# Kernel optimization log

Measured on AMD Instinct MI355X. Metric: run time of the kernel, lower is better.

Reference implementation:

```python
import jax, jax.numpy as jnp
import numpy as np

B, C, H, W = 4, 64, 64, 64
RATIO = 8  # channel reduction in the channel-attention branch
C8 = C // RATIO


def conv1x1(x, Wt, b):
    # 1x1 conv == channel-mixing matmul. Wt: (out_c, in_c), x: (B, in_c, H, W)
    return jnp.einsum('oc,bchw->bohw', Wt, x) + b[None, :, None, None]


def setup_inputs() -> dict:
    key = jax.random.key(0)
    ks = jax.random.split(key, 12)
    s = 0.02
    return {
        'x': jax.random.normal(ks[0], (B, C, H, W), dtype=jnp.float32),
        'y': jax.random.normal(ks[1], (B, C, H, W), dtype=jnp.float32),
        'Wq': jax.random.normal(ks[2], (C, C), dtype=jnp.float32) * s,
        'bq': jnp.zeros((C,), dtype=jnp.float32),
        'Wk': jax.random.normal(ks[3], (C, C), dtype=jnp.float32) * s,
        'bk': jnp.zeros((C,), dtype=jnp.float32),
        'Wv': jax.random.normal(ks[4], (C, C), dtype=jnp.float32) * s,
        'bv': jnp.zeros((C,), dtype=jnp.float32),
        'Wq1': jax.random.normal(ks[5], (C8, C), dtype=jnp.float32) * s,
        'bq1': jnp.zeros((C8,), dtype=jnp.float32),
        'Wk1': jax.random.normal(ks[6], (C8, C), dtype=jnp.float32) * s,
        'bk1': jnp.zeros((C8,), dtype=jnp.float32),
    }


def reference(x, y, Wq, bq, Wk, bk, Wv, bv, Wq1, bq1, Wk1, bk1):
    b, c, h, w = x.shape
    hw = h * w
    # cross-attention branch: query from y, key/value from x
    Q = conv1x1(y, Wq, bq).reshape(b, c, hw)   # (B, C, HW)
    K = conv1x1(x, Wk, bk).reshape(b, c, hw)
    V = conv1x1(x, Wv, bv).reshape(b, c, hw)
    attn = jax.nn.softmax(jnp.einsum('bcq,bck->bqk', Q, K), axis=-1)  # (B, HW, HW)
    # channel-attention branch (PAM-style spatial map from x, ratio 8)
    Q1 = conv1x1(x, Wq1, bq1).reshape(b, C8, hw)
    K1 = conv1x1(x, Wk1, bk1).reshape(b, C8, hw)
    attn1 = jax.nn.softmax(jnp.einsum('bcq,bck->bqk', Q1, K1), axis=-1)  # (B, HW, HW)
    # out = attn @ V^T + attn1 @ V^T, shape (B, HW, C)
    out = jnp.einsum('bqk,bck->bqc', attn, V) + jnp.einsum('bqk,bck->bqc', attn1, V)
    return out.transpose(0, 2, 1).reshape(b, c, h, w)
```

## Files before the change

kernel.cpp:

```cpp
#include <hip/hip_runtime.h>
#include <hip/hip_bf16.h>


typedef __bf16 bf16x8 __attribute__((ext_vector_type(8)));
typedef float f32x16 __attribute__((ext_vector_type(16)));

#define MFMA32(A, B, C) __builtin_amdgcn_mfma_f32_32x32x16_bf16((A), (B), (C), 0, 0, 0)

#define LOG2E 1.4426950408889634f
#define EXP2F(x) __builtin_amdgcn_exp2f(x)

__device__ __forceinline__ uint4 ld16(const unsigned short* p) {
  return *reinterpret_cast<const uint4*>(p);
}
__device__ __forceinline__ bf16x8 asbf(uint4 v) {
  return __builtin_bit_cast(bf16x8, v);
}
__device__ __forceinline__ unsigned short f2bf(float f) {
  return __builtin_bit_cast(unsigned short, __float2bfloat16(f));
}
__device__ __forceinline__ unsigned cvtpk(float a, float b) {
  unsigned r;
  asm("v_cvt_pk_bf16_f32 %0, %1, %2" : "=v"(r) : "v"(a), "v"(b));
  return r;
}

__global__ __launch_bounds__(256) void proj_kernel(
    const float* __restrict__ x, const float* __restrict__ y,
    const float* __restrict__ Wq, const float* __restrict__ bq,
    const float* __restrict__ Wk, const float* __restrict__ bk,
    const float* __restrict__ Wv, const float* __restrict__ bv,
    const float* __restrict__ Wq1, const float* __restrict__ bq1,
    const float* __restrict__ Wk1, const float* __restrict__ bk1,
    unsigned short* __restrict__ Qb, unsigned short* __restrict__ Kb,
    unsigned short* __restrict__ VtT, unsigned short* __restrict__ Q1c,
    unsigned short* __restrict__ K1c)
{
  __shared__ float ldsT[64][32];
  __shared__ float ldsW[64][65];
  __shared__ float ldsW2[64][65];
  __shared__ float ldsW1[8][64];
  __shared__ float ldsW1b[8][64];

  const int t = threadIdx.x;
  const int b = blockIdx.x >> 7;
  const int p0 = (blockIdx.x & 127) << 5;
  const int lane = t & 63;
  const int w = t >> 6;

  for (int i = t; i < 2048; i += 256) {
    int c = i >> 5, p = i & 31;
    ldsT[c][p] = y[(size_t)(b * 64 + c) * 4096 + p0 + p];
  }
  for (int i = t; i < 4096; i += 256) {
    int c = i >> 6, p = i & 63;
    ldsW[c][p] = Wq[i];
    ldsW2[c][p] = Wv[i];
  }
  for (int i = t; i < 512; i += 256) {
    ldsW1[i >> 6][i & 63] = Wq1[i];
    ldsW1b[i >> 6][i & 63] = Wk1[i];
  }
  __syncthreads();

  {
    float acc[8];
    float bias = bq[lane];
#pragma unroll
    for (int pp = 0; pp < 8; ++pp) acc[pp] = bias;
    for (int ic = 0; ic < 64; ++ic) {
      float wv_ = ldsW[lane][ic];
#pragma unroll
      for (int pp = 0; pp < 8; ++pp)
        acc[pp] = fmaf(wv_, ldsT[ic][w * 8 + pp], acc[pp]);
    }
#pragma unroll
    for (int pp = 0; pp < 8; ++pp)
      Qb[(size_t)(b * 4096 + p0 + w * 8 + pp) * 64 + lane] = f2bf(acc[pp] * LOG2E);
  }
  __syncthreads();

  for (int i = t; i < 2048; i += 256) {
    int c = i >> 5, p = i & 31;
    ldsT[c][p] = x[(size_t)(b * 64 + c) * 4096 + p0 + p];
  }
  for (int i = t; i < 4096; i += 256) {
    int c = i >> 6, p = i & 63;
    ldsW[c][p] = Wk[i];
  }
  __syncthreads();

  {
    float acc[8];
    float bias = bk[lane];
#pragma unroll
    for (int pp = 0; pp < 8; ++pp) acc[pp] = bias;
    for (int ic = 0; ic < 64; ++ic) {
      float wv_ = ldsW[lane][ic];
#pragma unroll
      for (int pp = 0; pp < 8; ++pp)
        acc[pp] = fmaf(wv_, ldsT[ic][w * 8 + pp], acc[pp]);
    }
#pragma unroll
    for (int pp = 0; pp < 8; ++pp)
      Kb[(size_t)(b * 4096 + p0 + w * 8 + pp) * 64 + lane] = f2bf(acc[pp]);
  }

  {
    const int half = lane >> 5;
    const int px = lane & 31;
    const int oc0 = 16 * w + 8 * half;
    float acc[8];
#pragma unroll
    for (int j = 0; j < 8; ++j) acc[j] = bv[oc0 + j];
    for (int ic = 0; ic < 64; ++ic) {
      float xv = ldsT[ic][px];
#pragma unroll
      for (int j = 0; j < 8; ++j)
        acc[j] = fmaf(ldsW2[oc0 + j][ic], xv, acc[j]);
    }
    const int k = p0 + px;
    const int kblk = k >> 5, ki = k & 31;
#pragma unroll
    for (int j = 0; j < 8; ++j)
      VtT[((size_t)(b * 128 + kblk) * 64 + oc0 + j) * 32 + ki] = f2bf(acc[j]);
  }

  if (w == 0 && lane < 32) {
    float acc[8];
#pragma unroll
    for (int j = 0; j < 8; ++j) acc[j] = bq1[j];
    for (int ic = 0; ic < 64; ++ic) {
      float xv = ldsT[ic][lane];
#pragma unroll
      for (int j = 0; j < 8; ++j)
        acc[j] = fmaf(ldsW1[j][ic], xv, acc[j]);
    }
    uint4 o;
    o.x = cvtpk(acc[0] * LOG2E, acc[1] * LOG2E);
    o.y = cvtpk(acc[2] * LOG2E, acc[3] * LOG2E);
    o.z = cvtpk(acc[4] * LOG2E, acc[5] * LOG2E);
    o.w = cvtpk(acc[6] * LOG2E, acc[7] * LOG2E);
    *reinterpret_cast<uint4*>(Q1c + (size_t)(b * 4096 + p0 + lane) * 8) = o;
  } else if (w == 1 && lane < 32) {
    float acc[8];
#pragma unroll
    for (int j = 0; j < 8; ++j) acc[j] = bk1[j];
    for (int ic = 0; ic < 64; ++ic) {
      float xv = ldsT[ic][lane];
#pragma unroll
      for (int j = 0; j < 8; ++j)
        acc[j] = fmaf(ldsW1b[j][ic], xv, acc[j]);
    }
    uint4 o;
    o.x = cvtpk(acc[0], acc[1]); o.y = cvtpk(acc[2], acc[3]);
    o.z = cvtpk(acc[4], acc[5]); o.w = cvtpk(acc[6], acc[7]);
    *reinterpret_cast<uint4*>(K1c + (size_t)(b * 4096 + p0 + lane) * 8) = o;
  }
}

__global__ __launch_bounds__(512, 2) void attn_kernel(
    const unsigned short* __restrict__ Qb, const unsigned short* __restrict__ Kb,
    const unsigned short* __restrict__ VtT, const unsigned short* __restrict__ Q1c,
    const unsigned short* __restrict__ K1c, float* __restrict__ out)
{
  __shared__ float accbuf[2][2][64][32];
  __shared__ float zbuf[8][2][32];

  const int id = blockIdx.x;
  const int b = (id & 7) >> 1;
  const int qt = (id >> 3) + ((id & 1) << 6);
  const int q0 = qt * 32;

  const int wid = threadIdx.x >> 6;
  const int l = threadIdx.x & 63;
  const int qc = l & 31;
  const int h = l >> 5;

  const int kBeg = wid << 9;
  const int kEnd = kBeg + 512;

  const f32x16 zero16 = {0.f,0.f,0.f,0.f, 0.f,0.f,0.f,0.f,
                         0.f,0.f,0.f,0.f, 0.f,0.f,0.f,0.f};
  const uint4 zu4 = {0u, 0u, 0u, 0u};

  const unsigned short* qrow = Qb + (size_t)(b * 4096 + q0 + qc) * 64 + 8 * h;
  bf16x8 qf[4];
#pragma unroll
  for (int m = 0; m < 4; ++m) qf[m] = asbf(ld16(qrow + 16 * m));
  bf16x8 q1f;
  {
    uint4 v = zu4;
    if (h == 0) v = ld16(Q1c + (size_t)(b * 4096 + q0 + qc) * 8);
    q1f = asbf(v);
  }

  f32x16 accA0 = zero16, accA1 = zero16, accB0 = zero16, accB1 = zero16;
  float zA = 0.f, zB = 0.f;

#pragma unroll 1
  for (int k0 = kBeg; k0 < kEnd; k0 += 32) {
    uint4 kf[4], vf[4], k1f;
    {
      const unsigned short* kp = Kb + ((size_t)(b * 4096 + k0 + qc) << 6) + 8 * h;
      kf[0] = ld16(kp);
      kf[1] = ld16(kp + 16);
      kf[2] = ld16(kp + 32);
      kf[3] = ld16(kp + 48);
      k1f = zu4;
      if (h == 0) k1f = ld16(K1c + (size_t)(b * 4096 + k0 + qc) * 8);
      const unsigned short* vp =
          VtT + (((size_t)(b * 128 + (k0 >> 5)) * 64 + qc) << 5) + 8 * h;
      vf[0] = ld16(vp);
      vf[1] = ld16(vp + 16);
      vf[2] = ld16(vp + 32 * 32);
      vf[3] = ld16(vp + 32 * 32 + 16);
    }

    __builtin_amdgcn_s_setprio(1);
    f32x16 sD = MFMA32(asbf(kf[0]), qf[0], zero16);
    sD = MFMA32(asbf(kf[1]), qf[1], sD);
    sD = MFMA32(asbf(kf[2]), qf[2], sD);
    sD = MFMA32(asbf(kf[3]), qf[3], sD);
    f32x16 uD = MFMA32(asbf(k1f), q1f, zero16);
    __builtin_amdgcn_s_setprio(0);

#pragma unroll
    for (int r = 0; r < 16; ++r) { sD[r] = EXP2F(sD[r]); uD[r] = EXP2F(uD[r]); }
    zA += (((sD[0]+sD[1])+(sD[2]+sD[3])) + ((sD[4]+sD[5])+(sD[6]+sD[7]))) +
          (((sD[8]+sD[9])+(sD[10]+sD[11])) + ((sD[12]+sD[13])+(sD[14]+sD[15])));
    zB += (((uD[0]+uD[1])+(uD[2]+uD[3])) + ((uD[4]+uD[5])+(uD[6]+uD[7]))) +
          (((uD[8]+uD[9])+(uD[10]+uD[11])) + ((uD[12]+uD[13])+(uD[14]+uD[15])));

#pragma unroll
    for (int m = 0; m < 2; ++m) {
      unsigned W0 = cvtpk(sD[8*m+0], sD[8*m+1]);
      unsigned W1 = cvtpk(sD[8*m+2], sD[8*m+3]);
      unsigned W2 = cvtpk(sD[8*m+4], sD[8*m+5]);
      unsigned W3 = cvtpk(sD[8*m+6], sD[8*m+7]);
      auto s1 = __builtin_amdgcn_permlane32_swap((int)W0, (int)W2, false, false);
      auto s2 = __builtin_amdgcn_permlane32_swap((int)W1, (int)W3, false, false);
      uint4 pw;
      pw.x = (unsigned)s1[0]; pw.y = (unsigned)s2[0];
      pw.z = (unsigned)s1[1]; pw.w = (unsigned)s2[1];
      bf16x8 pf = asbf(pw);

      unsigned X0 = cvtpk(uD[8*m+0], uD[8*m+1]);
      unsigned X1 = cvtpk(uD[8*m+2], uD[8*m+3]);
      unsigned X2 = cvtpk(uD[8*m+4], uD[8*m+5]);
      unsigned X3 = cvtpk(uD[8*m+6], uD[8*m+7]);
      auto t1 = __builtin_amdgcn_permlane32_swap((int)X0, (int)X2, false, false);
      auto t2 = __builtin_amdgcn_permlane32_swap((int)X1, (int)X3, false, false);
      uint4 pw1;
      pw1.x = (unsigned)t1[0]; pw1.y = (unsigned)t2[0];
      pw1.z = (unsigned)t1[1]; pw1.w = (unsigned)t2[1];
      bf16x8 pf1 = asbf(pw1);

      __builtin_amdgcn_s_setprio(1);
      accA0 = MFMA32(asbf(vf[m]),     pf,  accA0);
      accA1 = MFMA32(asbf(vf[2 + m]), pf,  accA1);
      accB0 = MFMA32(asbf(vf[m]),     pf1, accB0);
      accB1 = MFMA32(asbf(vf[2 + m]), pf1, accB1);
      __builtin_amdgcn_s_setprio(0);
    }
  }

  zA += __shfl_xor(zA, 32);
  zB += __shfl_xor(zB, 32);
  if (h == 0) { zbuf[wid][0][qc] = zA; zbuf[wid][1][qc] = zB; }

  auto payload_write = [&](int slot) {
#pragma unroll
    for (int r = 0; r < 16; ++r) {
      const int c0 = (r & 3) + 8 * (r >> 2) + 4 * h;
      accbuf[slot][0][c0][qc]      = accA0[r];
      accbuf[slot][0][c0 + 32][qc] = accA1[r];
      accbuf[slot][1][c0][qc]      = accB0[r];
      accbuf[slot][1][c0 + 32][qc] = accB1[r];
    }
  };
  auto payload_add = [&](int slot) {
#pragma unroll
    for (int r = 0; r < 16; ++r) {
      const int c0 = (r & 3) + 8 * (r >> 2) + 4 * h;
      accA0[r] += accbuf[slot][0][c0][qc];
      accA1[r] += accbuf[slot][0][c0 + 32][qc];
      accB0[r] += accbuf[slot][1][c0][qc];
      accB1[r] += accbuf[slot][1][c0 + 32][qc];
    }
  };

  if (wid == 1) payload_write(0);
  if (wid == 5) payload_write(1);
  __syncthreads();
  if (wid == 0) payload_add(0);
  if (wid == 4) payload_add(1);
  __syncthreads();
  if (wid == 3) payload_write(0);
  if (wid == 7) payload_write(1);
  __syncthreads();
  if (wid == 2) payload_add(0);
  if (wid == 6) payload_add(1);
  __syncthreads();
  if (wid == 2) payload_write(0);
  if (wid == 6) payload_write(1);
  __syncthreads();
  if (wid == 0) payload_add(0);
  if (wid == 4) payload_add(1);
  __syncthreads();
  if (wid == 4) payload_write(0);
  __syncthreads();
  if (wid == 0) {
    payload_add(0);
    float zAt = 0.f, zBt = 0.f;
#pragma unroll
    for (int ww = 0; ww < 8; ++ww) { zAt += zbuf[ww][0][qc]; zBt += zbuf[ww][1][qc]; }
    const float rA = 1.0f / zAt, rB = 1.0f / zBt;
    float* op = out + (size_t)b * (64 * 4096) + q0 + qc;
#pragma unroll
    for (int r = 0; r < 16; ++r) {
      const int c0 = (r & 3) + 8 * (r >> 2) + 4 * h;
      op[(size_t)c0 * 4096]        = accA0[r] * rA + accB0[r] * rB;
      op[(size_t)(c0 + 32) * 4096] = accA1[r] * rA + accB1[r] * rB;
    }
  }
}

extern "C" void kernel_launch(void* const* d_in, const int* in_sizes, int n_in,
                              void* d_out, int out_size, void* d_ws, size_t ws_size,
                              hipStream_t stream) {
  (void)in_sizes; (void)n_in; (void)out_size; (void)ws_size;
  const float* x = (const float*)d_in[0];
  const float* y = (const float*)d_in[1];
  const float* Wq = (const float*)d_in[2];
  const float* bq = (const float*)d_in[3];
  const float* Wk = (const float*)d_in[4];
  const float* bk = (const float*)d_in[5];
  const float* Wv = (const float*)d_in[6];
  const float* bv = (const float*)d_in[7];
  const float* Wq1 = (const float*)d_in[8];
  const float* bq1 = (const float*)d_in[9];
  const float* Wk1 = (const float*)d_in[10];
  const float* bk1 = (const float*)d_in[11];

  char* ws = (char*)d_ws;
  unsigned short* Qb = (unsigned short*)(ws);
  unsigned short* Kb = (unsigned short*)(ws + (2u << 20));
  unsigned short* VtT = (unsigned short*)(ws + (4u << 20));
  unsigned short* Q1c = (unsigned short*)(ws + (6u << 20));
  unsigned short* K1c = (unsigned short*)(ws + (6u << 20) + (256u << 10));

  proj_kernel<<<512, 256, 0, stream>>>(x, y, Wq, bq, Wk, bk, Wv, bv,
                                       Wq1, bq1, Wk1, bk1, Qb, Kb, VtT, Q1c, K1c);
  attn_kernel<<<512, 512, 0, stream>>>(Qb, Kb, VtT, Q1c, K1c, (float*)d_out);
}
```

Baseline: 79.48 us.

## Split attention waves across output-channel halves instead of eight key slices

Work in the attention kernel is now split between waves by output-channel half (32 channels each) and four key ranges, instead of eight key ranges covering all 64 channels. Each wave holds two accumulators instead of four, which cuts register pressure, and the launch hint moves to 4 waves per EU. The cross-wave reduction also shrinks to three barrier steps. In exchange, each QK^T score tile and its exp are computed twice, once per channel-half wave, so score and exp work doubles.

```diff
diff --git a/kernel.cpp b/kernel.cpp
--- a/kernel.cpp
+++ b/kernel.cpp
@@ -159,13 +159,15 @@
   }
 }
 
-__global__ __launch_bounds__(512, 2) void attn_kernel(
+__global__ __launch_bounds__(512)
+__attribute__((amdgpu_waves_per_eu(4)))
+void attn_kernel(
     const unsigned short* __restrict__ Qb, const unsigned short* __restrict__ Kb,
     const unsigned short* __restrict__ VtT, const unsigned short* __restrict__ Q1c,
     const unsigned short* __restrict__ K1c, float* __restrict__ out)
 {
-  __shared__ float accbuf[2][2][64][32];
-  __shared__ float zbuf[8][2][32];
+  __shared__ float accbuf[4][2][32][32];
+  __shared__ float zbuf[4][2][32];
 
   const int id = blockIdx.x;
   const int b = (id & 7) >> 1;
@@ -173,12 +175,14 @@
   const int q0 = qt * 32;
 
   const int wid = threadIdx.x >> 6;
+  const int ks = wid & 3;
+  const int ch = wid >> 2;
   const int l = threadIdx.x & 63;
   const int qc = l & 31;
   const int h = l >> 5;
 
-  const int kBeg = wid << 9;
-  const int kEnd = kBeg + 512;
+  const int kBeg = ks << 10;
+  const int kEnd = kBeg + 1024;
 
   const f32x16 zero16 = {0.f,0.f,0.f,0.f, 0.f,0.f,0.f,0.f,
                          0.f,0.f,0.f,0.f, 0.f,0.f,0.f,0.f};
@@ -195,12 +199,12 @@
     q1f = asbf(v);
   }
 
-  f32x16 accA0 = zero16, accA1 = zero16, accB0 = zero16, accB1 = zero16;
+  f32x16 accA = zero16, accB = zero16;
   float zA = 0.f, zB = 0.f;
 
 #pragma unroll 1
   for (int k0 = kBeg; k0 < kEnd; k0 += 32) {
-    uint4 kf[4], vf[4], k1f;
+    uint4 kf[4], vf[2], k1f;
     {
       const unsigned short* kp = Kb + ((size_t)(b * 4096 + k0 + qc) << 6) + 8 * h;
       kf[0] = ld16(kp);
@@ -210,11 +214,9 @@
       k1f = zu4;
       if (h == 0) k1f = ld16(K1c + (size_t)(b * 4096 + k0 + qc) * 8);
       const unsigned short* vp =
-          VtT + (((size_t)(b * 128 + (k0 >> 5)) * 64 + qc) << 5) + 8 * h;
+          VtT + (((size_t)(b * 128 + (k0 >> 5)) * 64 + ch * 32 + qc) << 5) + 8 * h;
       vf[0] = ld16(vp);
       vf[1] = ld16(vp + 16);
-      vf[2] = ld16(vp + 32 * 32);
-      vf[3] = ld16(vp + 32 * 32 + 16);
     }
 
     __builtin_amdgcn_s_setprio(1);
@@ -257,71 +259,50 @@
       bf16x8 pf1 = asbf(pw1);
 
       __builtin_amdgcn_s_setprio(1);
-      accA0 = MFMA32(asbf(vf[m]),     pf,  accA0);
-      accA1 = MFMA32(asbf(vf[2 + m]), pf,  accA1);
-      accB0 = MFMA32(asbf(vf[m]),     pf1, accB0);
-      accB1 = MFMA32(asbf(vf[2 + m]), pf1, accB1);
+      accA = MFMA32(asbf(vf[m]), pf,  accA);
+      accB = MFMA32(asbf(vf[m]), pf1, accB);
       __builtin_amdgcn_s_setprio(0);
     }
   }
 
   zA += __shfl_xor(zA, 32);
   zB += __shfl_xor(zB, 32);
-  if (h == 0) { zbuf[wid][0][qc] = zA; zbuf[wid][1][qc] = zB; }
+  if (ch == 0 && h == 0) { zbuf[ks][0][qc] = zA; zbuf[ks][1][qc] = zB; }
 
   auto payload_write = [&](int slot) {
 #pragma unroll
     for (int r = 0; r < 16; ++r) {
       const int c0 = (r & 3) + 8 * (r >> 2) + 4 * h;
-      accbuf[slot][0][c0][qc]      = accA0[r];
-      accbuf[slot][0][c0 + 32][qc] = accA1[r];
-      accbuf[slot][1][c0][qc]      = accB0[r];
-      accbuf[slot][1][c0 + 32][qc] = accB1[r];
+      accbuf[slot][0][c0][qc] = accA[r];
+      accbuf[slot][1][c0][qc] = accB[r];
     }
   };
   auto payload_add = [&](int slot) {
 #pragma unroll
     for (int r = 0; r < 16; ++r) {
       const int c0 = (r & 3) + 8 * (r >> 2) + 4 * h;
-      accA0[r] += accbuf[slot][0][c0][qc];
-      accA1[r] += accbuf[slot][0][c0 + 32][qc];
-      accB0[r] += accbuf[slot][1][c0][qc];
-      accB1[r] += accbuf[slot][1][c0 + 32][qc];
+      accA[r] += accbuf[slot][0][c0][qc];
+      accB[r] += accbuf[slot][1][c0][qc];
     }
   };
 
-  if (wid == 1) payload_write(0);
-  if (wid == 5) payload_write(1);
-  __syncthreads();
-  if (wid == 0) payload_add(0);
-  if (wid == 4) payload_add(1);
-  __syncthreads();
-  if (wid == 3) payload_write(0);
-  if (wid == 7) payload_write(1);
-  __syncthreads();
-  if (wid == 2) payload_add(0);
-  if (wid == 6) payload_add(1);
-  __syncthreads();
-  if (wid == 2) payload_write(0);
-  if (wid == 6) payload_write(1);
-  __syncthreads();
-  if (wid == 0) payload_add(0);
-  if (wid == 4) payload_add(1);
-  __syncthreads();
-  if (wid == 4) payload_write(0);
-  __syncthreads();
-  if (wid == 0) {
-    payload_add(0);
-    float zAt = 0.f, zBt = 0.f;
-#pragma unroll
-    for (int ww = 0; ww < 8; ++ww) { zAt += zbuf[ww][0][qc]; zBt += zbuf[ww][1][qc]; }
+  if (ks & 1) payload_write(ch * 2 + (ks >> 1));
+  __syncthreads();
+  if ((ks & 1) == 0) payload_add(ch * 2 + (ks >> 1));
+  __syncthreads();
+  if (ks == 2) payload_write(ch * 2);
+  __syncthreads();
+  if (ks == 0) {
+    payload_add(ch * 2);
+    const float zAt = zbuf[0][0][qc] + zbuf[1][0][qc] + zbuf[2][0][qc] + zbuf[3][0][qc];
+    const float zBt = zbuf[0][1][qc] + zbuf[1][1][qc] + zbuf[2][1][qc] + zbuf[3][1][qc];
     const float rA = 1.0f / zAt, rB = 1.0f / zBt;
     float* op = out + (size_t)b * (64 * 4096) + q0 + qc;
 #pragma unroll
     for (int r = 0; r < 16; ++r) {
       const int c0 = (r & 3) + 8 * (r >> 2) + 4 * h;
-      op[(size_t)c0 * 4096]        = accA0[r] * rA + accB0[r] * rB;
-      op[(size_t)(c0 + 32) * 4096] = accA1[r] * rA + accB1[r] * rB;
+      const int c = ch * 32 + c0;
+      op[(size_t)c * 4096] = accA[r] * rA + accB[r] * rB;
     }
   }
 }
```

Result: slower. 104.9 us (+32.0%).
